# Kernel optimization log

Measured on AMD Instinct MI355X. Metric: run time of the kernel, lower is better.

Reference implementation:

```python
import jax, jax.numpy as jnp
import numpy as np

K_TABLE = 8388608   # number of stored key/value pairs (2**23)
N_QUERY = 4194304   # number of lookups (2**22)
KEY_SPACE = 2147483647
DEFAULT_VALUE = -1  # DenseHashTable default_value for missing keys


def setup_inputs() -> dict:
    key = jax.random.key(0)
    k1, k2, k3, k4 = jax.random.split(key, 4)
    # Hash table contents, represented as a sorted key array + aligned values.
    table_keys = jnp.sort(jax.random.randint(k1, (K_TABLE,), 1, KEY_SPACE, dtype=jnp.int64))
    table_values = jax.random.randint(k2, (K_TABLE,), 0, 1000000, dtype=jnp.int64)
    # Queries: half random ids (mostly misses), half sampled from the table (hits).
    q_rand = jax.random.randint(k3, (N_QUERY // 2,), 1, KEY_SPACE, dtype=jnp.int64)
    hit_idx = jax.random.randint(k4, (N_QUERY // 2,), 0, K_TABLE, dtype=jnp.int64)
    q_hit = table_keys[hit_idx]
    query = jnp.concatenate([q_rand, q_hit])
    return {"query": query, "table_keys": table_keys, "table_values": table_values}


def reference(query, table_keys, table_values):
    # DenseHashTable.lookup: for each query id return its stored value,
    # or default_value (-1) if the key is absent. Implemented as a sorted
    # binary-search gather (same math: exact-match key -> value map).
    idx = jnp.searchsorted(table_keys, query)                 # [N]
    idx_c = jnp.clip(idx, 0, table_keys.shape[0] - 1)
    hit = table_keys[idx_c] == query                          # [N] bool
    out = jnp.where(hit, table_values[idx_c], jnp.int64(DEFAULT_VALUE))
    return out
```

## Files before the change

kernel.cpp:

```cpp
#include <hip/hip_runtime.h>


constexpr int SENTINEL = (int)0x80000000;

__global__ void build_table_kernel(const int* __restrict__ keys,
                                   const int* __restrict__ vals, int K,
                                   int4* __restrict__ table,
                                   int shift, unsigned B) {
    int i = blockIdx.x * blockDim.x + threadIdx.x;
    if (i >= K) return;
    unsigned b  = ((unsigned)keys[i]) >> shift;
    unsigned bn = (i + 1 < K) ? (((unsigned)keys[i + 1]) >> shift) : B;

    if (i == 0) {
        for (unsigned e = 0; e < b; ++e) table[e] = make_int4(0, 0, 0, 0);
    } else {
        unsigned bp = ((unsigned)keys[i - 1]) >> shift;
        if (bp != b) {
            for (unsigned e = bp + 1; e < b; ++e) table[e] = make_int4(0, 0, 0, 0);
        }
    }

    if (bn != b) {
        int first = i;
        while (first > 0 && (((unsigned)keys[first - 1]) >> shift) == b) --first;
        int cnt = i - first + 1;
        int4 e;
        if (cnt == 1)      e = make_int4(keys[i], vals[i], 0, 0);
        else if (cnt == 2) e = make_int4(keys[first], vals[first], keys[i], vals[i]);
        else               e = make_int4(SENTINEL, first, i + 1, 0);
        table[b] = e;
        if (i == K - 1) {
            for (unsigned t = b + 1; t < B; ++t) table[t] = make_int4(0, 0, 0, 0);
        }
    }
}

__global__ void lookup16_kernel(const int* __restrict__ query,
                                const int* __restrict__ keys,
                                const int* __restrict__ vals,
                                const int4* __restrict__ table,
                                int* __restrict__ out,
                                int N, int shift, unsigned Bmask) {
    int i = blockIdx.x * blockDim.x + threadIdx.x;
    if (i >= N) return;
    int q = query[i];
    int4 e = table[(((unsigned)q) >> shift) & Bmask];
    int r;
    if (e.x == q) {
        r = e.y;
    } else if (e.x == SENTINEL) {
        r = -1;
        int lo = e.y, hi = e.z;
        for (int j = lo; j < hi; ++j) {
            int k = keys[j];
            if (k >= q) { if (k == q) r = vals[j]; break; }
        }
    } else if (e.z == q) {
        r = e.w;
    } else {
        r = -1;
    }
    out[i] = r;
}

__global__ void lookup_bsearch_kernel(const int* __restrict__ query,
                                      const int* __restrict__ keys,
                                      const int* __restrict__ vals,
                                      int* __restrict__ out,
                                      int N, int K) {
    int i = blockIdx.x * blockDim.x + threadIdx.x;
    if (i >= N) return;
    int q = query[i];
    int lo = 0, hi = K;
    while (lo < hi) {
        int mid = (lo + hi) >> 1;
        if (keys[mid] < q) lo = mid + 1; else hi = mid;
    }
    int r = -1;
    if (lo < K && keys[lo] == q) r = vals[lo];
    out[i] = r;
}

extern "C" void kernel_launch(void* const* d_in, const int* in_sizes, int n_in,
                              void* d_out, int out_size, void* d_ws, size_t ws_size,
                              hipStream_t stream) {
    const int* query = (const int*)d_in[0];
    const int* keys  = (const int*)d_in[1];
    const int* vals  = (const int*)d_in[2];
    int* out = (int*)d_out;
    const int N = in_sizes[0];
    const int K = in_sizes[1];
    const int tb = 256;

    int logB = 23;
    while (logB > 18 && ((size_t)16 << logB) > ws_size) logB--;

    if (((size_t)16 << logB) <= ws_size) {
        unsigned B = 1u << logB;
        int shift = 31 - logB;
        int4* table = (int4*)d_ws;
        build_table_kernel<<<(K + tb - 1) / tb, tb, 0, stream>>>(keys, vals, K,
                                                                 table, shift, B);
        lookup16_kernel<<<(N + tb - 1) / tb, tb, 0, stream>>>(query, keys, vals,
                                                              table, out, N,
                                                              shift, B - 1);
    } else {
        lookup_bsearch_kernel<<<(N + tb - 1) / tb, tb, 0, stream>>>(query, keys, vals,
                                                                    out, N, K);
    }
}
```

Before: 166.9 us.

## Pack up to four key/value pairs per bucket with 8-bit key tags

Result: slower. 176.9 us (+6.0%).

```diff
diff --git a/kernel.cpp b/kernel.cpp
--- a/kernel.cpp
+++ b/kernel.cpp
@@ -2,6 +2,86 @@
 
 
 constexpr int SENTINEL = (int)0x80000000;
+
+
+__global__ void build_packed_kernel(const int* __restrict__ keys,
+                                    const int* __restrict__ vals, int K,
+                                    int4* __restrict__ table, unsigned B) {
+    int i = blockIdx.x * blockDim.x + threadIdx.x;
+    if (i >= K) return;
+    unsigned b = ((unsigned)keys[i]) >> 8;
+
+    if (i == 0) {
+        for (unsigned e = 0; e < b; ++e) table[e] = make_int4(0, 0, 0, 0);
+    } else {
+        unsigned bp = ((unsigned)keys[i - 1]) >> 8;
+        if (bp != b) {
+            for (unsigned e = bp + 1; e < b; ++e) table[e] = make_int4(0, 0, 0, 0);
+        }
+    }
+
+    unsigned bn = (i + 1 < K) ? (((unsigned)keys[i + 1]) >> 8) : 0xFFFFFFFFu;
+    if (bn != b) {
+        int first = i;
+        while (first > 0 && ((((unsigned)keys[first - 1]) >> 8) == b)) --first;
+        int cnt = i - first + 1;
+        int w[4] = {0, 0, 0, 0};
+        bool ok = (cnt <= 4);
+        if (ok) {
+            for (int j = 0; j < cnt; ++j) {
+                int v = vals[first + j];
+                if ((unsigned)v > 0xFFFFFu) { ok = false; break; }
+                w[j] = (1 << 28) | (v << 8) | (keys[first + j] & 0xFF);
+            }
+        }
+        int4 e = ok ? make_int4(w[0], w[1], w[2], w[3])
+                    : make_int4(2 << 28, first, i + 1, 0);
+        table[b] = e;
+        if (i == K - 1) {
+            for (unsigned t = b + 1; t < B; ++t) table[t] = make_int4(0, 0, 0, 0);
+        }
+    }
+}
+
+__device__ __forceinline__ int resolve_packed(int q, int4 e,
+                                              const int* __restrict__ keys,
+                                              const int* __restrict__ vals) {
+    if ((((unsigned)e.x) >> 28) == 2u) {
+        int r = -1;
+        for (int j = e.y; j < e.z; ++j) {
+            int k = keys[j];
+            if (k >= q) { if (k == q) r = vals[j]; break; }
+        }
+        return r;
+    }
+    int ql = q & 0xFF;
+    int w;
+    w = e.x; if ((((unsigned)w) >> 28) == 1u && (w & 0xFF) == ql) return (w >> 8) & 0xFFFFF;
+    w = e.y; if ((((unsigned)w) >> 28) == 1u && (w & 0xFF) == ql) return (w >> 8) & 0xFFFFF;
+    w = e.z; if ((((unsigned)w) >> 28) == 1u && (w & 0xFF) == ql) return (w >> 8) & 0xFFFFF;
+    w = e.w; if ((((unsigned)w) >> 28) == 1u && (w & 0xFF) == ql) return (w >> 8) & 0xFFFFF;
+    return -1;
+}
+
+__global__ void lookup_packed_kernel(const int* __restrict__ query,
+                                     const int* __restrict__ keys,
+                                     const int* __restrict__ vals,
+                                     const int4* __restrict__ table,
+                                     int* __restrict__ out,
+                                     int N, unsigned Bmask) {
+    int half = (N + 1) >> 1;
+    int i = blockIdx.x * blockDim.x + threadIdx.x;
+    if (i >= half) return;
+    int i1 = i + half;
+    bool has1 = (i1 < N);
+    int q0 = query[i];
+    int q1 = has1 ? query[i1] : q0;
+    int4 e0 = table[(((unsigned)q0) >> 8) & Bmask];
+    int4 e1 = table[(((unsigned)q1) >> 8) & Bmask];
+    out[i] = resolve_packed(q0, e0, keys, vals);
+    if (has1) out[i1] = resolve_packed(q1, e1, keys, vals);
+}
+
 
 __global__ void build_table_kernel(const int* __restrict__ keys,
                                    const int* __restrict__ vals, int K,
@@ -11,7 +91,6 @@
     if (i >= K) return;
     unsigned b  = ((unsigned)keys[i]) >> shift;
     unsigned bn = (i + 1 < K) ? (((unsigned)keys[i + 1]) >> shift) : B;
-
     if (i == 0) {
         for (unsigned e = 0; e < b; ++e) table[e] = make_int4(0, 0, 0, 0);
     } else {
@@ -20,7 +99,6 @@
             for (unsigned e = bp + 1; e < b; ++e) table[e] = make_int4(0, 0, 0, 0);
         }
     }
-
     if (bn != b) {
         int first = i;
         while (first > 0 && (((unsigned)keys[first - 1]) >> shift) == b) --first;
@@ -51,8 +129,7 @@
         r = e.y;
     } else if (e.x == SENTINEL) {
         r = -1;
-        int lo = e.y, hi = e.z;
-        for (int j = lo; j < hi; ++j) {
+        for (int j = e.y; j < e.z; ++j) {
             int k = keys[j];
             if (k >= q) { if (k == q) r = vals[j]; break; }
         }
@@ -93,20 +170,29 @@
     const int K = in_sizes[1];
     const int tb = 256;
 
-    int logB = 23;
-    while (logB > 18 && ((size_t)16 << logB) > ws_size) logB--;
-
-    if (((size_t)16 << logB) <= ws_size) {
-        unsigned B = 1u << logB;
-        int shift = 31 - logB;
+    if (((size_t)16 << 23) <= ws_size) {
+        unsigned B = 1u << 23;
         int4* table = (int4*)d_ws;
-        build_table_kernel<<<(K + tb - 1) / tb, tb, 0, stream>>>(keys, vals, K,
-                                                                 table, shift, B);
-        lookup16_kernel<<<(N + tb - 1) / tb, tb, 0, stream>>>(query, keys, vals,
-                                                              table, out, N,
-                                                              shift, B - 1);
+        build_packed_kernel<<<(K + tb - 1) / tb, tb, 0, stream>>>(keys, vals, K,
+                                                                  table, B);
+        int half = (N + 1) >> 1;
+        lookup_packed_kernel<<<(half + tb - 1) / tb, tb, 0, stream>>>(
+            query, keys, vals, table, out, N, B - 1);
     } else {
-        lookup_bsearch_kernel<<<(N + tb - 1) / tb, tb, 0, stream>>>(query, keys, vals,
-                                                                    out, N, K);
+        int logB = 22;
+        while (logB > 18 && ((size_t)16 << logB) > ws_size) logB--;
+        if (((size_t)16 << logB) <= ws_size) {
+            unsigned B = 1u << logB;
+            int shift = 31 - logB;
+            int4* table = (int4*)d_ws;
+            build_table_kernel<<<(K + tb - 1) / tb, tb, 0, stream>>>(keys, vals, K,
+                                                                     table, shift, B);
+            lookup16_kernel<<<(N + tb - 1) / tb, tb, 0, stream>>>(query, keys, vals,
+                                                                  table, out, N,
+                                                                  shift, B - 1);
+        } else {
+            lookup_bsearch_kernel<<<(N + tb - 1) / tb, tb, 0, stream>>>(query, keys,
+                                                                        vals, out, N, K);
+        }
     }
 }
```
